# Optimization experiments

Hardware: AMD Instinct MI355X
Metric: run time of the kernel (lower is better)

## Reference

```python
import jax, jax.numpy as jnp
import numpy as np

N_SH, N_U, N_I = 1195, 805, 390   # hard-coded in KDHR
D = 64                            # embedding_dim / latent_dim
B = 65536                         # prescription batch
E_SH = 100000
BN_EPS = 1e-5


def setup_inputs() -> dict:
    key = jax.random.key(0)
    ks = jax.random.split(key, 20)
    s = 0.02
    return {
        "edge_index_SH": jax.random.randint(ks[0], (2, E_SH), 0, N_SH),
        "edge_index_SS": jax.random.randint(ks[1], (2, 50000), 0, N_U),
        "edge_index_HH": jax.random.randint(ks[2], (2, 50000), 0, N_I),
        "prescription": jax.random.uniform(ks[3], (B, N_I), dtype=jnp.float32),
        "sh_emb": jax.random.normal(ks[4], (N_SH, D), dtype=jnp.float32) * s,
        # GCNConv_SH layer 1 and 2 (Linear weights, torch layout [out,in])
        "W1": jax.random.normal(ks[5], (D, D), dtype=jnp.float32) * s,
        "b1": jnp.zeros((D,), jnp.float32),
        "W2": jax.random.normal(ks[6], (D, D), dtype=jnp.float32) * s,
        "b2": jnp.zeros((D,), jnp.float32),
        # proj = Linear(64,64) -> ELU -> Linear(64,64)
        "Wp1": jax.random.normal(ks[7], (D, D), dtype=jnp.float32) * s,
        "bp1": jnp.zeros((D,), jnp.float32),
        "Wp2": jax.random.normal(ks[8], (D, D), dtype=jnp.float32) * s,
        "bp2": jnp.zeros((D,), jnp.float32),
        # self.mlp = Linear(64,64); self.SI_bn = BatchNorm1d(64)
        "Wm": jax.random.normal(ks[9], (D, D), dtype=jnp.float32) * s,
        "bm": jnp.zeros((D,), jnp.float32),
        "bn_gamma": jnp.ones((D,), jnp.float32),
        "bn_beta": jnp.zeros((D,), jnp.float32),
    }


def _gcn_layer(x, W, b, src, dst):
    # GCNConv_SH: message = lin(x_j), aggr='mean' at dst, then tanh
    m = x[src] @ W.T + b                                   # [E, D]
    s = jax.ops.segment_sum(m, dst, num_segments=N_SH)     # [N_SH, D]
    cnt = jax.ops.segment_sum(jnp.ones(dst.shape, x.dtype), dst, num_segments=N_SH)
    return jnp.tanh(s / jnp.maximum(cnt, 1.0)[:, None])


def _l2n(z):
    return z / jnp.linalg.norm(z, axis=1, keepdims=True)


def reference(edge_index_SH, edge_index_SS, edge_index_HH, prescription,
              sh_emb, W1, b1, W2, b2, Wp1, bp1, Wp2, bp2, Wm, bm,
              bn_gamma, bn_beta):
    src, dst = edge_index_SH[0], edge_index_SH[1]
    h1 = _gcn_layer(sh_emb, W1, b1, src, dst)
    h2 = _gcn_layer(h1, W2, b2, src, dst)                  # x_SH6
    c_emb_u, c_emb_i = h2[:N_U], h2[N_U:]                  # [805,64], [390,64]

    def proj(z):
        return jax.nn.elu(z @ Wp1.T + bp1) @ Wp2.T + bp2

    # Same2Loss projected+normalized embeddings (c_u: herbs 390, c_i: users 805)
    es = _l2n(proj(c_emb_i))                               # [390, 64]
    eh = _l2n(proj(c_emb_u))                               # [805, 64]

    e_synd = prescription @ es                             # [B, 64]
    pre_sum = jnp.sum(prescription, axis=1, keepdims=True)
    e = e_synd / pre_sum
    e = e @ Wm.T + bm                                      # mlp
    mu = jnp.mean(e, axis=0)                               # BatchNorm1d (train)
    var = jnp.var(e, axis=0)
    e = (e - mu) * jax.lax.rsqrt(var + BN_EPS) * bn_gamma + bn_beta
    e = jax.nn.relu(e)
    return e @ eh.T                                        # [B, 805]
```

## Files before the change

### kernel.cpp

```cpp
#include <hip/hip_runtime.h>
#include <math.h>

#define NSH 1195
#define NU  805
#define NI  390
#define DD  64
#define BROWS 65536
#define ESH 100000
#define KPAD 416
#define NUPAD 832

typedef _Float16 f16;
typedef _Float16 f16x8 __attribute__((ext_vector_type(8)));
typedef float f32x4 __attribute__((ext_vector_type(4)));

#define OFF_STATS  0u
#define OFF_ESWT   128u
#define OFF_EH     13440u
#define OFF_HIST   40064u
#define ZERO_FLOATS 41344u
#define OFF_ROWPTR 41344u
#define OFF_CURSOR 42624u
#define OFF_COLIDX 43904u
#define OFF_H1     144000u
#define OFF_EPRE   220480u

__global__ __launch_bounds__(256) void hist_kernel(const int* __restrict__ edges,
                                                   int* __restrict__ hist) {
    int e = blockIdx.x * 256 + threadIdx.x;
    if (e < ESH) atomicAdd(&hist[edges[ESH + e]], 1);
}

__global__ __launch_bounds__(1024) void scan_kernel(const int* __restrict__ hist,
                                                    int* __restrict__ row_ptr,
                                                    int* __restrict__ cursor) {
    __shared__ int s[2048];
    int t = threadIdx.x;
    s[t] = (t < NSH) ? hist[t] : 0;
    s[t + 1024] = (t + 1024 < NSH) ? hist[t + 1024] : 0;
    __syncthreads();
    for (int off = 1; off < 2048; off <<= 1) {
        int a = s[t], b = s[t + 1024];
        int aa = (t >= off) ? s[t - off] : 0;
        int bb = s[t + 1024 - off];
        __syncthreads();
        s[t] = a + aa;
        s[t + 1024] = b + bb;
        __syncthreads();
    }
    if (t == 0) row_ptr[0] = 0;
    for (int i = t; i < NSH; i += 1024) {
        row_ptr[i + 1] = s[i];
        cursor[i] = (i == 0) ? 0 : s[i - 1];
    }
}

__global__ __launch_bounds__(256) void scatter_kernel(const int* __restrict__ edges,
                                                      int* __restrict__ cursor,
                                                      int* __restrict__ col_idx) {
    int e = blockIdx.x * 256 + threadIdx.x;
    if (e < ESH) {
        int t = edges[ESH + e];
        int pos = atomicAdd(&cursor[t], 1);
        col_idx[pos] = edges[e];
    }
}

__global__ __launch_bounds__(256) void gcn_gather1(const int* __restrict__ row_ptr,
                                                   const int* __restrict__ col_idx,
                                                   const float* __restrict__ x,
                                                   const float* __restrict__ W,
                                                   const float* __restrict__ b,
                                                   float* __restrict__ out) {
    __shared__ float s_wt[DD * DD];
    __shared__ float s_p[4 * DD];
    int tid = threadIdx.x;
    int w = tid >> 6, lane = tid & 63;
    for (int i = tid; i < DD * DD; i += 256) {
        int j = i >> 6, k = i & 63;
        s_wt[k * DD + j] = W[i];
    }
    int node = blockIdx.x;
    int beg = row_ptr[node], end = row_ptr[node + 1];
    float acc = 0.f;
    for (int e = beg + w; e < end; e += 4)
        acc += x[col_idx[e] * DD + lane];
    s_p[w * DD + lane] = acc;
    __syncthreads();
    float z = s_p[lane] + s_p[DD + lane] + s_p[2 * DD + lane] + s_p[3 * DD + lane];
    __syncthreads();
    if (w == 0) s_p[lane] = z;
    __syncthreads();
    float cntf = (float)(end - beg);
    float o = cntf * b[lane];
    #pragma unroll 8
    for (int k = 0; k < DD; k++)
        o = fmaf(s_p[k], s_wt[k * DD + lane], o);
    float h = tanhf(o / fmaxf(cntf, 1.f));
    if (w == 0) out[node * DD + lane] = h;
}

__global__ __launch_bounds__(256) void gcn2_fused(const int* __restrict__ row_ptr,
                                                  const int* __restrict__ col_idx,
                                                  const float* __restrict__ h1,
                                                  const float* __restrict__ W2,
                                                  const float* __restrict__ b2,
                                                  const float* __restrict__ Wp1,
                                                  const float* __restrict__ bp1,
                                                  const float* __restrict__ Wp2,
                                                  const float* __restrict__ bp2,
                                                  const float* __restrict__ Wm,
                                                  f16* __restrict__ eh16,
                                                  f16* __restrict__ esWT) {
    __shared__ float s_w2[DD * DD], s_p1[DD * DD], s_p2[DD * DD], s_wm[DD * DD];
    __shared__ float s_v[4 * DD];
    int tid = threadIdx.x;
    int w = tid >> 6, lane = tid & 63;
    for (int i = tid; i < DD * DD; i += 256) {
        int j = i >> 6, k = i & 63;
        s_w2[k * DD + j] = W2[i];
        s_p1[k * DD + j] = Wp1[i];
        s_p2[k * DD + j] = Wp2[i];
        s_wm[k * DD + j] = Wm[i];
    }
    int node = blockIdx.x;
    int beg = row_ptr[node], end = row_ptr[node + 1];
    float acc = 0.f;
    for (int e = beg + w; e < end; e += 4)
        acc += h1[col_idx[e] * DD + lane];
    s_v[w * DD + lane] = acc;
    __syncthreads();
    float z = s_v[lane] + s_v[DD + lane] + s_v[2 * DD + lane] + s_v[3 * DD + lane];
    __syncthreads();
    if (w == 0) s_v[lane] = z;
    __syncthreads();
    float cntf = (float)(end - beg);
    float o = cntf * b2[lane];
    #pragma unroll 8
    for (int k = 0; k < DD; k++)
        o = fmaf(s_v[k], s_w2[k * DD + lane], o);
    float h2v = tanhf(o / fmaxf(cntf, 1.f));
    __syncthreads();
    if (w == 0) s_v[lane] = h2v;
    __syncthreads();
    float t = bp1[lane];
    #pragma unroll 8
    for (int k = 0; k < DD; k++)
        t = fmaf(s_v[k], s_p1[k * DD + lane], t);
    t = t > 0.f ? t : expm1f(t);
    __syncthreads();
    if (w == 0) s_v[lane] = t;
    __syncthreads();
    float o2 = bp2[lane];
    #pragma unroll 8
    for (int k = 0; k < DD; k++)
        o2 = fmaf(s_v[k], s_p2[k * DD + lane], o2);
    float sq = o2 * o2;
    #pragma unroll
    for (int off = 1; off < 64; off <<= 1) sq += __shfl_xor(sq, off);
    float r = o2 / sqrtf(sq);
    if (node < NU) {
        if (w == 0) eh16[node * DD + lane] = (f16)r;
    } else {
        __syncthreads();
        if (w == 0) s_v[lane] = r;
        __syncthreads();
        float m = 0.f;
        #pragma unroll 8
        for (int k = 0; k < DD; k++)
            m = fmaf(s_v[k], s_wm[k * DD + lane], m);
        if (w == 0) esWT[lane * KPAD + (node - NU)] = (f16)m;
    }
}

__global__ __launch_bounds__(256) void synd_mfma(const float* __restrict__ P,
                                                 const f16* __restrict__ esWT,
                                                 const float* __restrict__ bm,
                                                 float* __restrict__ e_pre,
                                                 float* __restrict__ stats) {
    __shared__ float s_stats[128];
    int tid = threadIdx.x;
    if (tid < 128) s_stats[tid] = 0.f;
    __syncthreads();
    int lane = tid & 63, wv = tid >> 6;
    int l15 = lane & 15, lk = lane >> 4;
    int rowbase = blockIdx.x * 128 + wv * 32;

    f32x4 acc[2][4];
    #pragma unroll
    for (int mi = 0; mi < 2; mi++)
        #pragma unroll
        for (int ni = 0; ni < 4; ni++)
            acc[mi][ni] = (f32x4){0.f, 0.f, 0.f, 0.f};
    float rs[2] = {0.f, 0.f};

    const float* pr[2];
    pr[0] = P + (size_t)(rowbase + l15) * NI;
    pr[1] = P + (size_t)(rowbase + 16 + l15) * NI;
    const f16* bp[4];
    #pragma unroll
    for (int ni = 0; ni < 4; ni++)
        bp[ni] = esWT + (size_t)(ni * 16 + l15) * KPAD;

    for (int step = 0; step < 12; step++) {
        int kb = step * 32 + lk * 8;
        f16x8 afr[2];
        #pragma unroll
        for (int mi = 0; mi < 2; mi++) {
            const float* p = pr[mi] + kb;
            float2 q0 = *(const float2*)(p);
            float2 q1 = *(const float2*)(p + 2);
            float2 q2 = *(const float2*)(p + 4);
            float2 q3 = *(const float2*)(p + 6);
            rs[mi] += ((q0.x + q0.y) + (q1.x + q1.y)) + ((q2.x + q2.y) + (q3.x + q3.y));
            f16x8 a;
            a[0] = (f16)q0.x; a[1] = (f16)q0.y; a[2] = (f16)q1.x; a[3] = (f16)q1.y;
            a[4] = (f16)q2.x; a[5] = (f16)q2.y; a[6] = (f16)q3.x; a[7] = (f16)q3.y;
            afr[mi] = a;
        }
        f16x8 bfr[4];
        #pragma unroll
        for (int ni = 0; ni < 4; ni++)
            bfr[ni] = *(const f16x8*)(bp[ni] + kb);
        #pragma unroll
        for (int mi = 0; mi < 2; mi++)
            #pragma unroll
            for (int ni = 0; ni < 4; ni++)
                acc[mi][ni] = __builtin_amdgcn_mfma_f32_16x16x32_f16(
                    afr[mi], bfr[ni], acc[mi][ni], 0, 0, 0);
    }
    {
        f16x8 afr[2];
        #pragma unroll
        for (int mi = 0; mi < 2; mi++) {
            f16x8 a = (f16x8)(f16)0.f;
            if (lk == 0) {
                const float* p = pr[mi] + 384;
                float2 q0 = *(const float2*)(p);
                float2 q1 = *(const float2*)(p + 2);
                float2 q2 = *(const float2*)(p + 4);
                rs[mi] += ((q0.x + q0.y) + (q1.x + q1.y)) + (q2.x + q2.y);
                a[0] = (f16)q0.x; a[1] = (f16)q0.y; a[2] = (f16)q1.x;
                a[3] = (f16)q1.y; a[4] = (f16)q2.x; a[5] = (f16)q2.y;
            }
            afr[mi] = a;
        }
        f16x8 bfr[4];
        #pragma unroll
        for (int ni = 0; ni < 4; ni++)
            bfr[ni] = *(const f16x8*)(bp[ni] + 384 + lk * 8);
        #pragma unroll
        for (int mi = 0; mi < 2; mi++)
            #pragma unroll
            for (int ni = 0; ni < 4; ni++)
                acc[mi][ni] = __builtin_amdgcn_mfma_f32_16x16x32_f16(
                    afr[mi], bfr[ni], acc[mi][ni], 0, 0, 0);
    }

    #pragma unroll
    for (int mi = 0; mi < 2; mi++) {
        rs[mi] += __shfl_xor(rs[mi], 16);
        rs[mi] += __shfl_xor(rs[mi], 32);
    }
    float rsr[2][4];
    #pragma unroll
    for (int mi = 0; mi < 2; mi++)
        #pragma unroll
        for (int j = 0; j < 4; j++)
            rsr[mi][j] = __shfl(rs[mi], lk * 4 + j);

    float bmv[4];
    #pragma unroll
    for (int ni = 0; ni < 4; ni++) bmv[ni] = bm[ni * 16 + l15];

    #pragma unroll
    for (int ni = 0; ni < 4; ni++) {
        float s = 0.f, q = 0.f;
        #pragma unroll
        for (int mi = 0; mi < 2; mi++) {
            #pragma unroll
            for (int j = 0; j < 4; j++) {
                float v = acc[mi][ni][j] / rsr[mi][j] + bmv[ni];
                int row = rowbase + mi * 16 + lk * 4 + j;
                e_pre[(size_t)row * DD + ni * 16 + l15] = v;
                s += v;
                q = fmaf(v, v, q);
            }
        }
        s += __shfl_xor(s, 16); s += __shfl_xor(s, 32);
        q += __shfl_xor(q, 16); q += __shfl_xor(q, 32);
        if (lk == 0) {
            atomicAdd(&s_stats[ni * 16 + l15], s);
            atomicAdd(&s_stats[64 + ni * 16 + l15], q);
        }
    }
    __syncthreads();
    if (tid < 128) atomicAdd(&stats[tid], s_stats[tid]);
}

#define CG0 448
__global__ __launch_bounds__(256) void out_fused(const float* __restrict__ e_pre,
                                                 const f16* __restrict__ eh16,
                                                 const float* __restrict__ stats,
                                                 const float* __restrict__ gamma,
                                                 const float* __restrict__ beta,
                                                 float* __restrict__ out) {
    __shared__ __align__(16) f16 s_eh[CG0 * DD];
    __shared__ float s_bn[128];
    int tid = threadIdx.x;
    int cg = blockIdx.x;
    int nrows = cg == 0 ? CG0 : (NUPAD - CG0);
    int cbase = cg * CG0;

    if (tid < 64) {
        float mu  = stats[tid] * (1.0f / 65536.0f);
        float ex2 = stats[64 + tid] * (1.0f / 65536.0f);
        float var = ex2 - mu * mu;
        float rstd = 1.0f / sqrtf(var + 1e-5f);
        float sc = rstd * gamma[tid];
        s_bn[tid] = sc;
        s_bn[64 + tid] = beta[tid] - mu * sc;
    }

    const uint4* src = (const uint4*)(eh16 + (size_t)cbase * DD);
    int nchunks = nrows * 8;
    for (int c = tid; c < nchunks; c += 256) {
        int row = c >> 3, slot = c & 7;
        uint4 v = src[c];
        *(uint4*)&s_eh[row * DD + ((slot ^ (row & 7)) << 3)] = v;
    }
    __syncthreads();

    int lane = tid & 63, w = tid >> 6;
    int l15 = lane & 15, lk = lane >> 4;
    int r0 = blockIdx.y * 64 + w * 16;

    f16x8 afr[2];
    {
        const float* pr = e_pre + (size_t)(r0 + l15) * DD;
        #pragma unroll
        for (int ks = 0; ks < 2; ks++) {
            int kb = ks * 32 + lk * 8;
            f32x4 v0 = *(const f32x4*)&pr[kb];
            f32x4 v1 = *(const f32x4*)&pr[kb + 4];
            f16x8 a;
            #pragma unroll
            for (int i = 0; i < 4; i++) {
                a[i]     = (f16)fmaxf(fmaf(v0[i], s_bn[kb + i],     s_bn[64 + kb + i]),     0.f);
                a[4 + i] = (f16)fmaxf(fmaf(v1[i], s_bn[kb + 4 + i], s_bn[64 + kb + 4 + i]), 0.f);
            }
            afr[ks] = a;
        }
    }

    int nt = cg == 0 ? 7 : 6;
    for (int cb = 0; cb < nt; cb += 4) {
        f32x4 acc[4][4];
        #pragma unroll
        for (int tt = 0; tt < 4; tt++)
            #pragma unroll
            for (int c16 = 0; c16 < 4; c16++)
                acc[tt][c16] = (f32x4){0.f, 0.f, 0.f, 0.f};

        #pragma unroll
        for (int tt = 0; tt < 4; tt++) {
            if (cb + tt < nt) {
                #pragma unroll
                for (int c16 = 0; c16 < 4; c16++) {
                    int lc = (cb + tt) * 64 + c16 * 16 + l15;
                    #pragma unroll
                    for (int ks = 0; ks < 2; ks++) {
                        int slot = (ks * 4 + lk) ^ (lc & 7);
                        f16x8 b = *(const f16x8*)&s_eh[lc * DD + (slot << 3)];
                        acc[tt][c16] = __builtin_amdgcn_mfma_f32_16x16x32_f16(
                            afr[ks], b, acc[tt][c16], 0, 0, 0);
                    }
                }
            }
        }
        #pragma unroll
        for (int tt = 0; tt < 4; tt++) {
            if (cb + tt < nt) {
                #pragma unroll
                for (int c16 = 0; c16 < 4; c16++) {
                    int col = cbase + (cb + tt) * 64 + c16 * 16 + l15;
                    if (col < NU) {
                        #pragma unroll
                        for (int j = 0; j < 4; j++) {
                            int row = r0 + lk * 4 + j;
                            out[(size_t)row * NU + col] = acc[tt][c16][j];
                        }
                    }
                }
            }
        }
    }
}

extern "C" void kernel_launch(void* const* d_in, const int* in_sizes, int n_in,
                              void* d_out, int out_size, void* d_ws, size_t ws_size,
                              hipStream_t stream) {
    const int*   eSH   = (const int*)d_in[0];
    const float* presc = (const float*)d_in[3];
    const float* shemb = (const float*)d_in[4];
    const float* W1  = (const float*)d_in[5];
    const float* b1  = (const float*)d_in[6];
    const float* W2  = (const float*)d_in[7];
    const float* b2  = (const float*)d_in[8];
    const float* Wp1 = (const float*)d_in[9];
    const float* bp1 = (const float*)d_in[10];
    const float* Wp2 = (const float*)d_in[11];
    const float* bp2 = (const float*)d_in[12];
    const float* Wm  = (const float*)d_in[13];
    const float* bm  = (const float*)d_in[14];
    const float* gam = (const float*)d_in[15];
    const float* bet = (const float*)d_in[16];

    float* ws    = (float*)d_ws;
    float* stats = ws + OFF_STATS;
    f16*   esWT  = (f16*)(ws + OFF_ESWT);
    f16*   eh16  = (f16*)(ws + OFF_EH);
    int*   hist  = (int*)(ws + OFF_HIST);
    int*   rowp  = (int*)(ws + OFF_ROWPTR);
    int*   curs  = (int*)(ws + OFF_CURSOR);
    int*   cidx  = (int*)(ws + OFF_COLIDX);
    float* h1    = ws + OFF_H1;
    float* e_pre = ws + OFF_EPRE;
    float* out   = (float*)d_out;

    hipMemsetAsync(ws, 0, ZERO_FLOATS * sizeof(float), stream);

    hist_kernel<<<391, 256, 0, stream>>>(eSH, hist);
    scan_kernel<<<1, 1024, 0, stream>>>(hist, rowp, curs);
    scatter_kernel<<<391, 256, 0, stream>>>(eSH, curs, cidx);
    gcn_gather1<<<NSH, 256, 0, stream>>>(rowp, cidx, shemb, W1, b1, h1);
    gcn2_fused<<<NSH, 256, 0, stream>>>(rowp, cidx, h1, W2, b2,
                                        Wp1, bp1, Wp2, bp2, Wm, eh16, esWT);
    synd_mfma<<<512, 256, 0, stream>>>(presc, esWT, bm, e_pre, stats);
    out_fused<<<dim3(2, 1024), 256, 0, stream>>>(e_pre, eh16, stats, gam, bet, out);
}
```

Measured before the change: 231.0 us.

## Stage prescription tile in LDS with coalesced loads and split output columns

The syndrome GEMM now loads each 64-row prescription tile with coalesced float4 reads, converts it to f16 into shared memory, and feeds MFMA from LDS. The row sums come from an extra MFMA against a ones vector instead of shuffle reductions. The output kernel splits the 805 columns into four groups instead of two, which lowers shared memory per block and per-thread accumulator registers but re-reads e_pre more often. Row sums are now accumulated from f16-rounded values, which slightly changes numerics.

```diff
diff --git a/kernel.cpp b/kernel.cpp
--- a/kernel.cpp
+++ b/kernel.cpp
@@ -11,6 +11,7 @@
 #define NUPAD 832
 
 typedef _Float16 f16;
+typedef _Float16 f16x2 __attribute__((ext_vector_type(2)));
 typedef _Float16 f16x8 __attribute__((ext_vector_type(8)));
 typedef float f32x4 __attribute__((ext_vector_type(4)));
 
@@ -173,101 +174,65 @@
     }
 }
 
-__global__ __launch_bounds__(256) void synd_mfma(const float* __restrict__ P,
-                                                 const f16* __restrict__ esWT,
-                                                 const float* __restrict__ bm,
-                                                 float* __restrict__ e_pre,
-                                                 float* __restrict__ stats) {
+__global__ __launch_bounds__(256) void synd_v2(const float* __restrict__ P,
+                                               const f16* __restrict__ esWT,
+                                               const float* __restrict__ bm,
+                                               float* __restrict__ e_pre,
+                                               float* __restrict__ stats) {
+    __shared__ __align__(16) f16 s_P[64 * KPAD];
     __shared__ float s_stats[128];
     int tid = threadIdx.x;
     if (tid < 128) s_stats[tid] = 0.f;
-    __syncthreads();
-    int lane = tid & 63, wv = tid >> 6;
+
+    for (int i = tid; i < 64 * 13; i += 256) {
+        int row = i / 13, j = i - row * 13;
+        *(uint32_t*)&s_P[row * KPAD + 390 + j * 2] = 0u;
+    }
+    const float* Pb = P + (size_t)blockIdx.x * 64 * NI;
+    for (int it = 0; it < 25; it++) {
+        int f = it * 1024 + tid * 4;
+        if (f < 64 * NI) {
+            f32x4 v = *(const f32x4*)(Pb + f);
+            int row = f / NI;
+            int col = f - row * NI;
+            *(f16x2*)&s_P[row * KPAD + col] = (f16x2){(f16)v.x, (f16)v.y};
+            int row2 = row, col2 = col + 2;
+            if (col2 == NI) { row2 = row + 1; col2 = 0; }
+            *(f16x2*)&s_P[row2 * KPAD + col2] = (f16x2){(f16)v.z, (f16)v.w};
+        }
+    }
+    __syncthreads();
+
+    int lane = tid & 63, w = tid >> 6;
     int l15 = lane & 15, lk = lane >> 4;
-    int rowbase = blockIdx.x * 128 + wv * 32;
-
-    f32x4 acc[2][4];
-    #pragma unroll
-    for (int mi = 0; mi < 2; mi++)
-        #pragma unroll
-        for (int ni = 0; ni < 4; ni++)
-            acc[mi][ni] = (f32x4){0.f, 0.f, 0.f, 0.f};
-    float rs[2] = {0.f, 0.f};
-
-    const float* pr[2];
-    pr[0] = P + (size_t)(rowbase + l15) * NI;
-    pr[1] = P + (size_t)(rowbase + 16 + l15) * NI;
+    int rowbase = blockIdx.x * 64 + w * 16;
+
+    f32x4 acc[5];
+    #pragma unroll
+    for (int ni = 0; ni < 5; ni++) acc[ni] = (f32x4){0.f, 0.f, 0.f, 0.f};
+
+    f16x8 ones;
+    #pragma unroll
+    for (int i = 0; i < 8; i++) ones[i] = (f16)1.0f;
+
+    const f16* arow = &s_P[(w * 16 + l15) * KPAD];
     const f16* bp[4];
     #pragma unroll
     for (int ni = 0; ni < 4; ni++)
         bp[ni] = esWT + (size_t)(ni * 16 + l15) * KPAD;
 
-    for (int step = 0; step < 12; step++) {
+    for (int step = 0; step < 13; step++) {
         int kb = step * 32 + lk * 8;
-        f16x8 afr[2];
-        #pragma unroll
-        for (int mi = 0; mi < 2; mi++) {
-            const float* p = pr[mi] + kb;
-            float2 q0 = *(const float2*)(p);
-            float2 q1 = *(const float2*)(p + 2);
-            float2 q2 = *(const float2*)(p + 4);
-            float2 q3 = *(const float2*)(p + 6);
-            rs[mi] += ((q0.x + q0.y) + (q1.x + q1.y)) + ((q2.x + q2.y) + (q3.x + q3.y));
-            f16x8 a;
-            a[0] = (f16)q0.x; a[1] = (f16)q0.y; a[2] = (f16)q1.x; a[3] = (f16)q1.y;
-            a[4] = (f16)q2.x; a[5] = (f16)q2.y; a[6] = (f16)q3.x; a[7] = (f16)q3.y;
-            afr[mi] = a;
-        }
+        f16x8 a = *(const f16x8*)(arow + kb);
         f16x8 bfr[4];
         #pragma unroll
         for (int ni = 0; ni < 4; ni++)
             bfr[ni] = *(const f16x8*)(bp[ni] + kb);
         #pragma unroll
-        for (int mi = 0; mi < 2; mi++)
-            #pragma unroll
-            for (int ni = 0; ni < 4; ni++)
-                acc[mi][ni] = __builtin_amdgcn_mfma_f32_16x16x32_f16(
-                    afr[mi], bfr[ni], acc[mi][ni], 0, 0, 0);
-    }
-    {
-        f16x8 afr[2];
-        #pragma unroll
-        for (int mi = 0; mi < 2; mi++) {
-            f16x8 a = (f16x8)(f16)0.f;
-            if (lk == 0) {
-                const float* p = pr[mi] + 384;
-                float2 q0 = *(const float2*)(p);
-                float2 q1 = *(const float2*)(p + 2);
-                float2 q2 = *(const float2*)(p + 4);
-                rs[mi] += ((q0.x + q0.y) + (q1.x + q1.y)) + (q2.x + q2.y);
-                a[0] = (f16)q0.x; a[1] = (f16)q0.y; a[2] = (f16)q1.x;
-                a[3] = (f16)q1.y; a[4] = (f16)q2.x; a[5] = (f16)q2.y;
-            }
-            afr[mi] = a;
-        }
-        f16x8 bfr[4];
-        #pragma unroll
         for (int ni = 0; ni < 4; ni++)
-            bfr[ni] = *(const f16x8*)(bp[ni] + 384 + lk * 8);
-        #pragma unroll
-        for (int mi = 0; mi < 2; mi++)
-            #pragma unroll
-            for (int ni = 0; ni < 4; ni++)
-                acc[mi][ni] = __builtin_amdgcn_mfma_f32_16x16x32_f16(
-                    afr[mi], bfr[ni], acc[mi][ni], 0, 0, 0);
-    }
-
-    #pragma unroll
-    for (int mi = 0; mi < 2; mi++) {
-        rs[mi] += __shfl_xor(rs[mi], 16);
-        rs[mi] += __shfl_xor(rs[mi], 32);
-    }
-    float rsr[2][4];
-    #pragma unroll
-    for (int mi = 0; mi < 2; mi++)
-        #pragma unroll
-        for (int j = 0; j < 4; j++)
-            rsr[mi][j] = __shfl(rs[mi], lk * 4 + j);
+            acc[ni] = __builtin_amdgcn_mfma_f32_16x16x32_f16(a, bfr[ni], acc[ni], 0, 0, 0);
+        acc[4] = __builtin_amdgcn_mfma_f32_16x16x32_f16(a, ones, acc[4], 0, 0, 0);
+    }
 
     float bmv[4];
     #pragma unroll
@@ -277,15 +242,12 @@
     for (int ni = 0; ni < 4; ni++) {
         float s = 0.f, q = 0.f;
         #pragma unroll
-        for (int mi = 0; mi < 2; mi++) {
-            #pragma unroll
-            for (int j = 0; j < 4; j++) {
-                float v = acc[mi][ni][j] / rsr[mi][j] + bmv[ni];
-                int row = rowbase + mi * 16 + lk * 4 + j;
-                e_pre[(size_t)row * DD + ni * 16 + l15] = v;
-                s += v;
-                q = fmaf(v, v, q);
-            }
+        for (int j = 0; j < 4; j++) {
+            float v = acc[ni][j] / acc[4][j] + bmv[ni];
+            int row = rowbase + lk * 4 + j;
+            e_pre[(size_t)row * DD + ni * 16 + l15] = v;
+            s += v;
+            q = fmaf(v, v, q);
         }
         s += __shfl_xor(s, 16); s += __shfl_xor(s, 32);
         q += __shfl_xor(q, 16); q += __shfl_xor(q, 32);
@@ -298,19 +260,20 @@
     if (tid < 128) atomicAdd(&stats[tid], s_stats[tid]);
 }
 
-#define CG0 448
 __global__ __launch_bounds__(256) void out_fused(const float* __restrict__ e_pre,
                                                  const f16* __restrict__ eh16,
                                                  const float* __restrict__ stats,
                                                  const float* __restrict__ gamma,
                                                  const float* __restrict__ beta,
                                                  float* __restrict__ out) {
-    __shared__ __align__(16) f16 s_eh[CG0 * DD];
+    __shared__ __align__(16) f16 s_eh[256 * DD];
     __shared__ float s_bn[128];
     int tid = threadIdx.x;
     int cg = blockIdx.x;
-    int nrows = cg == 0 ? CG0 : (NUPAD - CG0);
-    int cbase = cg * CG0;
+    int t0 = (cg == 0) ? 0 : cg * 3 + 1;
+    int nt = (cg == 0) ? 4 : 3;
+    int cbase = t0 * 64;
+    int nrows = nt * 64;
 
     if (tid < 64) {
         float mu  = stats[tid] * (1.0f / 65536.0f);
@@ -353,44 +316,28 @@
         }
     }
 
-    int nt = cg == 0 ? 7 : 6;
-    for (int cb = 0; cb < nt; cb += 4) {
-        f32x4 acc[4][4];
-        #pragma unroll
-        for (int tt = 0; tt < 4; tt++)
+    for (int tt = 0; tt < nt; tt++) {
+        f32x4 acc[4];
+        #pragma unroll
+        for (int c16 = 0; c16 < 4; c16++) acc[c16] = (f32x4){0.f, 0.f, 0.f, 0.f};
+        #pragma unroll
+        for (int c16 = 0; c16 < 4; c16++) {
+            int lc = tt * 64 + c16 * 16 + l15;
             #pragma unroll
-            for (int c16 = 0; c16 < 4; c16++)
-                acc[tt][c16] = (f32x4){0.f, 0.f, 0.f, 0.f};
-
-        #pragma unroll
-        for (int tt = 0; tt < 4; tt++) {
-            if (cb + tt < nt) {
+            for (int ks = 0; ks < 2; ks++) {
+                int slot = (ks * 4 + lk) ^ (lc & 7);
+                f16x8 b = *(const f16x8*)&s_eh[lc * DD + (slot << 3)];
+                acc[c16] = __builtin_amdgcn_mfma_f32_16x16x32_f16(afr[ks], b, acc[c16], 0, 0, 0);
+            }
+        }
+        #pragma unroll
+        for (int c16 = 0; c16 < 4; c16++) {
+            int col = cbase + tt * 64 + c16 * 16 + l15;
+            if (col < NU) {
                 #pragma unroll
-                for (int c16 = 0; c16 < 4; c16++) {
-                    int lc = (cb + tt) * 64 + c16 * 16 + l15;
-                    #pragma unroll
-                    for (int ks = 0; ks < 2; ks++) {
-                        int slot = (ks * 4 + lk) ^ (lc & 7);
-                        f16x8 b = *(const f16x8*)&s_eh[lc * DD + (slot << 3)];
-                        acc[tt][c16] = __builtin_amdgcn_mfma_f32_16x16x32_f16(
-                            afr[ks], b, acc[tt][c16], 0, 0, 0);
-                    }
-                }
-            }
-        }
-        #pragma unroll
-        for (int tt = 0; tt < 4; tt++) {
-            if (cb + tt < nt) {
-                #pragma unroll
-                for (int c16 = 0; c16 < 4; c16++) {
-                    int col = cbase + (cb + tt) * 64 + c16 * 16 + l15;
-                    if (col < NU) {
-                        #pragma unroll
-                        for (int j = 0; j < 4; j++) {
-                            int row = r0 + lk * 4 + j;
-                            out[(size_t)row * NU + col] = acc[tt][c16][j];
-                        }
-                    }
+                for (int j = 0; j < 4; j++) {
+                    int row = r0 + lk * 4 + j;
+                    out[(size_t)row * NU + col] = acc[c16][j];
                 }
             }
         }
@@ -436,6 +383,6 @@
     gcn_gather1<<<NSH, 256, 0, stream>>>(rowp, cidx, shemb, W1, b1, h1);
     gcn2_fused<<<NSH, 256, 0, stream>>>(rowp, cidx, h1, W2, b2,
                                         Wp1, bp1, Wp2, bp2, Wm, eh16, esWT);
-    synd_mfma<<<512, 256, 0, stream>>>(presc, esWT, bm, e_pre, stats);
-    out_fused<<<dim3(2, 1024), 256, 0, stream>>>(e_pre, eh16, stats, gam, bet, out);
-}
+    synd_v2<<<1024, 256, 0, stream>>>(presc, esWT, bm, e_pre, stats);
+    out_fused<<<dim3(4, 1024), 256, 0, stream>>>(e_pre, eh16, stats, gam, bet, out);
+}
```

After: 230.7 us. About the same (-0.1%).
